# Kernel optimization log

Measured on AMD Instinct MI355X. Metric: run time of the kernel, lower is better.

## Reference

```python
import jax, jax.numpy as jnp
import numpy as np
import math

D_MODEL = 2048
N_HEADS = 16
HEAD_DIM = D_MODEL // N_HEADS  # 128
SEQ = 2048
BATCH = 1


def make_freqs(seq_len, head_dim, theta=10000.0):
    # standard rotary frequencies: freqs_cis = exp(i * t * inv_freq)
    inv_freq = 1.0 / (theta ** (np.arange(0, head_dim, 2, dtype=np.float32) / head_dim))
    t = np.arange(seq_len, dtype=np.float32)
    ang = np.outer(t, inv_freq)  # [seq, head_dim/2]
    return jnp.asarray(np.cos(ang)), jnp.asarray(np.sin(ang))


def setup_inputs() -> dict:
    key = jax.random.key(0)
    ks = jax.random.split(key, 6)
    x = jax.random.normal(ks[0], (BATCH, SEQ, D_MODEL), dtype=jnp.float32)
    freqs_cos, freqs_sin = make_freqs(SEQ, HEAD_DIM)
    # causal additive mask, broadcastable to [b, h, s, s]
    mask = jnp.where(jnp.tril(jnp.ones((SEQ, SEQ), dtype=bool)), 0.0, -1e9).astype(jnp.float32)[None, None]
    scale = 0.02
    wq = jax.random.normal(ks[1], (D_MODEL, D_MODEL), dtype=jnp.float32) * scale
    wk = jax.random.normal(ks[2], (D_MODEL, D_MODEL), dtype=jnp.float32) * scale
    wv = jax.random.normal(ks[3], (D_MODEL, D_MODEL), dtype=jnp.float32) * scale
    wo = jax.random.normal(ks[4], (D_MODEL, D_MODEL), dtype=jnp.float32) * scale
    return {"x": x, "freqs_cos": freqs_cos, "freqs_sin": freqs_sin, "mask": mask,
            "wq": wq, "wk": wk, "wv": wv, "wo": wo}


def _apply_rotary(q, k, cos, sin):
    # q, k: [b, s, h, hd]; cos/sin: [s, hd/2]
    def rot(t):
        tr = t.reshape(*t.shape[:-1], -1, 2)  # [b, s, h, hd/2, 2]
        re, im = tr[..., 0], tr[..., 1]
        c = cos[None, :, None, :]
        s = sin[None, :, None, :]
        # complex multiply (re + i im) * (c + i s)
        out_re = re * c - im * s
        out_im = re * s + im * c
        return jnp.stack([out_re, out_im], axis=-1).reshape(t.shape)
    return rot(q), rot(k)


def reference(x, freqs_cos, freqs_sin, mask, wq, wk, wv, wo):
    b, s, _ = x.shape
    # QKV projections (nn.Linear with no bias: x @ W^T; W is square so use x @ W
    # with W stored already-transposed -- weights here are random so x @ W is faithful math)
    q = (x @ wq).reshape(b, s, N_HEADS, HEAD_DIM)
    k = (x @ wk).reshape(b, s, N_HEADS, HEAD_DIM)
    v = (x @ wv).reshape(b, s, N_HEADS, HEAD_DIM)
    q, k = _apply_rotary(q, k, freqs_cos, freqs_sin)
    # [b, h, s_q, s_k]
    scores = jnp.einsum("bqhd,bkhd->bhqk", q, k) / math.sqrt(HEAD_DIM)
    scores = scores + mask
    probs = jax.nn.softmax(scores.astype(jnp.float32), axis=-1).astype(q.dtype)
    out = jnp.einsum("bhqk,bkhd->bqhd", probs, v).reshape(b, s, N_HEADS * HEAD_DIM)
    return out @ wo
```

## Files before the change

### kernel.cpp

```cpp
#include <hip/hip_runtime.h>
#include <hip/hip_bf16.h>
#include <math.h>

#define SEQ 2048
#define DM 2048
#define NH 16
#define HD 128
#define QKV_N 6144

typedef __bf16 bf16;
typedef __bf16 bf16x8 __attribute__((ext_vector_type(8)));
typedef __bf16 bf16x4v __attribute__((ext_vector_type(4)));
typedef __bf16 bf16x2v __attribute__((ext_vector_type(2)));
typedef float f32x4 __attribute__((ext_vector_type(4)));

__device__ inline int sw_idx32(int row, int quad) {
    return (row * 4 + (quad ^ ((row >> 1) & 3))) * 8;
}
__device__ inline int sw_idx64(int row, int chunk) {
    return (row * 8 + (chunk ^ (row & 7))) * 8;
}

__device__ inline void async16(const void* g, void* l) {
    __builtin_amdgcn_global_load_lds((const __attribute__((address_space(1))) void*)g,
                                     (__attribute__((address_space(3))) void*)l, 16, 0, 0);
}

__global__ void k_prep(const float* __restrict__ wq, const float* __restrict__ wk,
                       const float* __restrict__ wv, const float* __restrict__ wo,
                       bf16* __restrict__ wT, bf16* __restrict__ woT,
                       const float* __restrict__ x, bf16* __restrict__ xb) {
    const int z = blockIdx.z;
    int tx = threadIdx.x, ty = threadIdx.y;
    if (z == 4) {
        int bid = blockIdx.y * 64 + blockIdx.x;
        if (bid >= 1024) return;
        int i = bid * 1024 + ty * 32 + tx;
        float4 v = ((const float4*)x)[i];
        bf16x4v o;
        o.x = (bf16)v.x; o.y = (bf16)v.y; o.z = (bf16)v.z; o.w = (bf16)v.w;
        ((bf16x4v*)xb)[i] = o;
        return;
    }
    __shared__ float tile[32][33];
    const float* src = (z == 0) ? wq : (z == 1) ? wk : (z == 2) ? wv : wo;
    bf16* dst = (z < 3) ? (wT + (size_t)z * DM * DM) : woT;
    int bx = blockIdx.x * 32, by = blockIdx.y * 32;
    tile[ty][tx] = src[(size_t)(by + ty) * DM + bx + tx];
    __syncthreads();
    dst[(size_t)(bx + ty) * DM + by + tx] = (bf16)tile[tx][ty];
}

__global__ void k_post(bf16* __restrict__ qkv, const float* __restrict__ cosT,
                       const float* __restrict__ sinT, bf16* __restrict__ vT) {
    __shared__ bf16 tile[32][33];
    int tx = threadIdx.x, ty = threadIdx.y;
    if (blockIdx.y < 64) {
        int bx = blockIdx.x * 32, by = blockIdx.y * 32;
        tile[ty][tx] = qkv[(size_t)(by + ty) * QKV_N + 2 * DM + bx + tx];
        __syncthreads();
        vT[(size_t)(bx + ty) * SEQ + by + tx] = tile[tx][ty];
    } else {
        int b = (blockIdx.y - 64) * 64 + blockIdx.x;
        int idx = b * 1024 + ty * 32 + tx;
        int i = idx & 63;
        int h = (idx >> 6) & 15;
        int s = idx >> 10;
        float c = cosT[s * 64 + i], sn = sinT[s * 64 + i];
        size_t base = (size_t)s * QKV_N + h * HD + 2 * i;
        bf16x2v q = *(bf16x2v*)&qkv[base];
        float qr = (float)q.x, qi = (float)q.y;
        bf16x2v qo;
        qo.x = (bf16)(qr * c - qi * sn);
        qo.y = (bf16)(qr * sn + qi * c);
        *(bf16x2v*)&qkv[base] = qo;
        bf16x2v k = *(bf16x2v*)&qkv[base + DM];
        float kr = (float)k.x, ki = (float)k.y;
        bf16x2v ko;
        ko.x = (bf16)(kr * c - ki * sn);
        ko.y = (bf16)(kr * sn + ki * c);
        *(bf16x2v*)&qkv[base + DM] = ko;
    }
}

template <typename OutT, int KSPLIT>
__global__ __launch_bounds__(256) void k_gemm_bt(const bf16* __restrict__ A,
                                                 const bf16* __restrict__ Bt,
                                                 OutT* __restrict__ C,
                                                 int M, int N, int K) {
    __shared__ bf16 As[128 * 64];
    __shared__ bf16 Bs[128 * 64];
    const int t = threadIdx.x;
    const int lane = t & 63;
    const int w = t >> 6;
    const int wr = (w >> 1) * 64, wc = (w & 1) * 64;
    const int l15 = lane & 15, quad = lane >> 4;
    const size_t bm = (size_t)blockIdx.y * 128, bn = (size_t)blockIdx.x * 128;
    const int Kb = K / KSPLIT;
    const int k0 = (KSPLIT > 1) ? (int)blockIdx.z * Kb : 0;
    f32x4 acc[4][4];
#pragma unroll
    for (int i = 0; i < 4; ++i)
#pragma unroll
        for (int j = 0; j < 4; ++j) acc[i][j] = (f32x4){0.f, 0.f, 0.f, 0.f};

    int srow[4], sgc[4];
#pragma unroll
    for (int j = 0; j < 4; ++j) {
        int c = j * 256 + t;
        srow[j] = c >> 3;
        sgc[j] = ((c & 7) ^ (srow[j] & 7)) * 8;
    }

    for (int kt = 0; kt < Kb; kt += 64) {
#pragma unroll
        for (int j = 0; j < 4; ++j) {
            async16(&A[(bm + srow[j]) * K + k0 + kt + sgc[j]], &As[(j * 256 + t) * 8]);
            async16(&Bt[(bn + srow[j]) * K + k0 + kt + sgc[j]], &Bs[(j * 256 + t) * 8]);
        }
        __syncthreads();
#pragma unroll
        for (int kh = 0; kh < 2; ++kh) {
            bf16x8 af[4], bfm[4];
#pragma unroll
            for (int mi = 0; mi < 4; ++mi)
                af[mi] = *(const bf16x8*)&As[sw_idx64(wr + mi * 16 + l15, kh * 4 + quad)];
#pragma unroll
            for (int ni = 0; ni < 4; ++ni)
                bfm[ni] = *(const bf16x8*)&Bs[sw_idx64(wc + ni * 16 + l15, kh * 4 + quad)];
#pragma unroll
            for (int mi = 0; mi < 4; ++mi)
#pragma unroll
                for (int ni = 0; ni < 4; ++ni)
                    acc[mi][ni] = __builtin_amdgcn_mfma_f32_16x16x32_bf16(
                        af[mi], bfm[ni], acc[mi][ni], 0, 0, 0);
        }
        __syncthreads();
    }
#pragma unroll
    for (int mi = 0; mi < 4; ++mi)
#pragma unroll
        for (int ni = 0; ni < 4; ++ni)
#pragma unroll
            for (int r = 0; r < 4; ++r) {
                size_t row = bm + wr + mi * 16 + quad * 4 + r;
                size_t col = bn + wc + ni * 16 + l15;
                if (KSPLIT > 1)
                    unsafeAtomicAdd((float*)&C[row * (size_t)N + col],
                                    (float)acc[mi][ni][r]);
                else
                    C[row * (size_t)N + col] = (OutT)acc[mi][ni][r];
            }
}

__global__ __launch_bounds__(256) void k_flash(const bf16* __restrict__ qkv,
                                               const bf16* __restrict__ vT,
                                               bf16* __restrict__ out) {
    __shared__ bf16 Ks[4][64 * 32];
    __shared__ bf16 Vs[2][128 * 32];
    __shared__ bf16 Pl[4][16][72];
    const int t = threadIdx.x;
    const int lane = t & 63;
    const int w = t >> 6;
    const int l15 = lane & 15, quad = lane >> 4;
    const int b = blockIdx.x;
    const int h = (b & 7) * 2 + ((b >> 3) & 1);
    const int qb = 31 - (b >> 4);
    const int q0w = qb * 64 + w * 16;
    const float sc = 0.08838834764831845f;

    const size_t qrow = (size_t)(q0w + l15) * QKV_N + h * HD;
    bf16x8 aq[4];
#pragma unroll
    for (int u = 0; u < 4; ++u)
        aq[u] = *(const bf16x8*)&qkv[qrow + u * 32 + quad * 8];

    f32x4 o[8];
#pragma unroll
    for (int c = 0; c < 8; ++c) o[c] = (f32x4){0.f, 0.f, 0.f, 0.f};
    float l_r[4] = {0.f, 0.f, 0.f, 0.f};

    const int srow = t >> 2;
    const int ch = ((t & 3) ^ ((t >> 3) & 3)) * 8;

    for (int kt = 0; kt <= qb; ++kt) {
        const int kbase = kt * 64;
#pragma unroll
        for (int u = 0; u < 4; ++u)
            async16(&qkv[(size_t)(kbase + srow) * QKV_N + DM + h * HD + u * 32 + ch],
                    &Ks[u][t * 8]);
#pragma unroll
        for (int j = 0; j < 2; ++j) {
            async16(&vT[(size_t)(h * HD + srow) * SEQ + kbase + j * 32 + ch],
                    &Vs[j][t * 8]);
            async16(&vT[(size_t)(h * HD + 64 + srow) * SEQ + kbase + j * 32 + ch],
                    &Vs[j][(t + 256) * 8]);
        }
        __syncthreads();
        f32x4 s[4];
#pragma unroll
        for (int sub = 0; sub < 4; ++sub) {
            f32x4 z = (f32x4){0.f, 0.f, 0.f, 0.f};
#pragma unroll
            for (int u = 0; u < 4; ++u) {
                bf16x8 kb = *(const bf16x8*)&Ks[u][sw_idx32(sub * 16 + l15, quad)];
                z = __builtin_amdgcn_mfma_f32_16x16x32_bf16(aq[u], kb, z, 0, 0, 0);
            }
            s[sub] = z;
        }
        const bool masked = (kt == qb);
#pragma unroll
        for (int sub = 0; sub < 4; ++sub)
#pragma unroll
            for (int r = 0; r < 4; ++r) {
                float p = __expf(s[sub][r] * sc);
                if (masked)
                    p = (kbase + sub * 16 + l15 <= q0w + quad * 4 + r) ? p : 0.f;
                l_r[r] += p;
                Pl[w][quad * 4 + r][sub * 16 + l15] = (bf16)p;
            }
        __syncthreads();
        bf16x8 pf0 = *(const bf16x8*)&Pl[w][l15][quad * 8];
        bf16x8 pf1 = *(const bf16x8*)&Pl[w][l15][32 + quad * 8];
#pragma unroll
        for (int c = 0; c < 8; ++c) {
            bf16x8 vb0 = *(const bf16x8*)&Vs[0][sw_idx32(c * 16 + l15, quad)];
            o[c] = __builtin_amdgcn_mfma_f32_16x16x32_bf16(pf0, vb0, o[c], 0, 0, 0);
            bf16x8 vb1 = *(const bf16x8*)&Vs[1][sw_idx32(c * 16 + l15, quad)];
            o[c] = __builtin_amdgcn_mfma_f32_16x16x32_bf16(pf1, vb1, o[c], 0, 0, 0);
        }
        __syncthreads();
    }

    float rl[4];
#pragma unroll
    for (int r = 0; r < 4; ++r) {
        float l = l_r[r];
        l += __shfl_xor(l, 1, 16);
        l += __shfl_xor(l, 2, 16);
        l += __shfl_xor(l, 4, 16);
        l += __shfl_xor(l, 8, 16);
        rl[r] = 1.0f / l;
    }
#pragma unroll
    for (int c = 0; c < 8; ++c)
#pragma unroll
        for (int r = 0; r < 4; ++r)
            out[(size_t)(q0w + quad * 4 + r) * DM + h * HD + c * 16 + l15] =
                (bf16)(o[c][r] * rl[r]);
}

extern "C" void kernel_launch(void* const* d_in, const int* in_sizes, int n_in,
                              void* d_out, int out_size, void* d_ws, size_t ws_size,
                              hipStream_t stream) {
    const float* x  = (const float*)d_in[0];
    const float* fc = (const float*)d_in[1];
    const float* fs = (const float*)d_in[2];
    const float* wq = (const float*)d_in[4];
    const float* wk = (const float*)d_in[5];
    const float* wv = (const float*)d_in[6];
    const float* wo = (const float*)d_in[7];
    float* out = (float*)d_out;

    char* ws = (char*)d_ws;
    bf16* xb  = (bf16*)(ws);
    bf16* wT  = (bf16*)(ws + (size_t)(8u  << 20));
    bf16* woT = (bf16*)(ws + (size_t)(32u << 20));
    bf16* qkv = (bf16*)(ws + (size_t)(40u << 20));
    bf16* vT  = (bf16*)(ws + (size_t)(64u << 20));

    hipMemsetAsync(out, 0, (size_t)SEQ * DM * sizeof(float), stream);
    k_prep<<<dim3(64, 64, 5), dim3(32, 32), 0, stream>>>(wq, wk, wv, wo, wT, woT, x, xb);
    k_gemm_bt<bf16, 1><<<dim3(48, 16), 256, 0, stream>>>(xb, wT, qkv, SEQ, QKV_N, DM);
    k_post<<<dim3(64, 96), dim3(32, 32), 0, stream>>>(qkv, fc, fs, vT);
    k_flash<<<512, 256, 0, stream>>>(qkv, vT, xb);
    k_gemm_bt<float, 2><<<dim3(16, 16, 2), 256, 0, stream>>>(xb, woT, out, SEQ, DM, DM);
}
```

Measured before the change: 331.1 us.

## Fuse rotary and V transpose into QKV GEMM epilogue; drop split-K output GEMM

The QKV projection GEMM now applies rotary embedding to Q/K in its epilogue, pairing adjacent columns with a lane shuffle. It also writes V transposed through a swizzled LDS staging tile, which removes the separate k_post kernel and its extra pass over qkv. The output projection drops split-K with atomics and the memset in favour of a 128x64 tile with direct stores and more blocks. In exchange the epilogue is heavier, and the output GEMM does a full-K loop per block with less reuse.

```diff
diff --git a/kernel.cpp b/kernel.cpp
--- a/kernel.cpp
+++ b/kernel.cpp
@@ -51,53 +51,22 @@
     dst[(size_t)(bx + ty) * DM + by + tx] = (bf16)tile[tx][ty];
 }
 
-__global__ void k_post(bf16* __restrict__ qkv, const float* __restrict__ cosT,
-                       const float* __restrict__ sinT, bf16* __restrict__ vT) {
-    __shared__ bf16 tile[32][33];
-    int tx = threadIdx.x, ty = threadIdx.y;
-    if (blockIdx.y < 64) {
-        int bx = blockIdx.x * 32, by = blockIdx.y * 32;
-        tile[ty][tx] = qkv[(size_t)(by + ty) * QKV_N + 2 * DM + bx + tx];
-        __syncthreads();
-        vT[(size_t)(bx + ty) * SEQ + by + tx] = tile[tx][ty];
-    } else {
-        int b = (blockIdx.y - 64) * 64 + blockIdx.x;
-        int idx = b * 1024 + ty * 32 + tx;
-        int i = idx & 63;
-        int h = (idx >> 6) & 15;
-        int s = idx >> 10;
-        float c = cosT[s * 64 + i], sn = sinT[s * 64 + i];
-        size_t base = (size_t)s * QKV_N + h * HD + 2 * i;
-        bf16x2v q = *(bf16x2v*)&qkv[base];
-        float qr = (float)q.x, qi = (float)q.y;
-        bf16x2v qo;
-        qo.x = (bf16)(qr * c - qi * sn);
-        qo.y = (bf16)(qr * sn + qi * c);
-        *(bf16x2v*)&qkv[base] = qo;
-        bf16x2v k = *(bf16x2v*)&qkv[base + DM];
-        float kr = (float)k.x, ki = (float)k.y;
-        bf16x2v ko;
-        ko.x = (bf16)(kr * c - ki * sn);
-        ko.y = (bf16)(kr * sn + ki * c);
-        *(bf16x2v*)&qkv[base + DM] = ko;
-    }
-}
-
-template <typename OutT, int KSPLIT>
-__global__ __launch_bounds__(256) void k_gemm_bt(const bf16* __restrict__ A,
-                                                 const bf16* __restrict__ Bt,
-                                                 OutT* __restrict__ C,
-                                                 int M, int N, int K) {
-    __shared__ bf16 As[128 * 64];
-    __shared__ bf16 Bs[128 * 64];
+__global__ __launch_bounds__(256) void k_gemm_qkv(const bf16* __restrict__ A,
+                                                  const bf16* __restrict__ Bt,
+                                                  bf16* __restrict__ qkv,
+                                                  bf16* __restrict__ vT,
+                                                  const float* __restrict__ cosT,
+                                                  const float* __restrict__ sinT) {
+    const int K = DM;
+    __shared__ bf16 smem[2 * 128 * 64];
+    bf16* As = smem;
+    bf16* Bs = smem + 128 * 64;
     const int t = threadIdx.x;
     const int lane = t & 63;
     const int w = t >> 6;
     const int wr = (w >> 1) * 64, wc = (w & 1) * 64;
     const int l15 = lane & 15, quad = lane >> 4;
     const size_t bm = (size_t)blockIdx.y * 128, bn = (size_t)blockIdx.x * 128;
-    const int Kb = K / KSPLIT;
-    const int k0 = (KSPLIT > 1) ? (int)blockIdx.z * Kb : 0;
     f32x4 acc[4][4];
 #pragma unroll
     for (int i = 0; i < 4; ++i)
@@ -112,11 +81,11 @@
         sgc[j] = ((c & 7) ^ (srow[j] & 7)) * 8;
     }
 
-    for (int kt = 0; kt < Kb; kt += 64) {
+    for (int kt = 0; kt < K; kt += 64) {
 #pragma unroll
         for (int j = 0; j < 4; ++j) {
-            async16(&A[(bm + srow[j]) * K + k0 + kt + sgc[j]], &As[(j * 256 + t) * 8]);
-            async16(&Bt[(bn + srow[j]) * K + k0 + kt + sgc[j]], &Bs[(j * 256 + t) * 8]);
+            async16(&A[(bm + srow[j]) * K + kt + sgc[j]], &As[(j * 256 + t) * 8]);
+            async16(&Bt[(bn + srow[j]) * K + kt + sgc[j]], &Bs[(j * 256 + t) * 8]);
         }
         __syncthreads();
 #pragma unroll
@@ -137,19 +106,112 @@
         }
         __syncthreads();
     }
+
+    if (blockIdx.x < 32) {
+        const bool is_re = (l15 & 1) == 0;
+#pragma unroll
+        for (int mi = 0; mi < 4; ++mi)
+#pragma unroll
+            for (int ni = 0; ni < 4; ++ni) {
+                const int n_local = wc + ni * 16 + l15;
+                const int i = n_local >> 1;
+#pragma unroll
+                for (int r = 0; r < 4; ++r) {
+                    size_t row = bm + wr + mi * 16 + quad * 4 + r;
+                    float c = cosT[row * 64 + i];
+                    float sn = sinT[row * 64 + i];
+                    float a = acc[mi][ni][r];
+                    float p = __shfl_xor(a, 1);
+                    float v = is_re ? (a * c - p * sn) : (p * sn + a * c);
+                    qkv[row * QKV_N + bn + n_local] = (bf16)v;
+                }
+            }
+    } else {
+#pragma unroll
+        for (int mi = 0; mi < 4; ++mi)
+#pragma unroll
+            for (int ni = 0; ni < 4; ++ni) {
+                const int n_local = wc + ni * 16 + l15;
+#pragma unroll
+                for (int r = 0; r < 4; ++r) {
+                    int s_local = wr + mi * 16 + quad * 4 + r;
+                    smem[n_local * 128 + ((((s_local >> 3) ^ (n_local & 15)) * 8) |
+                                          (s_local & 7))] = (bf16)acc[mi][ni][r];
+                }
+            }
+        __syncthreads();
+        const int n_l = t >> 1;
+        const size_t ch = bn - 4096 + n_l;
+#pragma unroll
+        for (int j = 0; j < 8; ++j) {
+            int c = (t & 1) * 8 + j;
+            bf16x8 v = *(const bf16x8*)&smem[n_l * 128 + ((c ^ (n_l & 15)) * 8)];
+            *(bf16x8*)&vT[ch * SEQ + bm + c * 8] = v;
+        }
+    }
+}
+
+template <typename OutT, int BN>
+__global__ __launch_bounds__(256) void k_gemm_bt(const bf16* __restrict__ A,
+                                                 const bf16* __restrict__ Bt,
+                                                 OutT* __restrict__ C,
+                                                 int M, int N, int K) {
+    constexpr int NI = BN / 32;
+    __shared__ bf16 As[128 * 64];
+    __shared__ bf16 Bs[BN * 64];
+    const int t = threadIdx.x;
+    const int lane = t & 63;
+    const int w = t >> 6;
+    const int wr = (w >> 1) * 64, wc = (w & 1) * (BN / 2);
+    const int l15 = lane & 15, quad = lane >> 4;
+    const size_t bm = (size_t)blockIdx.y * 128, bn = (size_t)blockIdx.x * BN;
+    f32x4 acc[4][NI];
+#pragma unroll
+    for (int i = 0; i < 4; ++i)
+#pragma unroll
+        for (int j = 0; j < NI; ++j) acc[i][j] = (f32x4){0.f, 0.f, 0.f, 0.f};
+
+    for (int kt = 0; kt < K; kt += 64) {
+#pragma unroll
+        for (int j = 0; j < 4; ++j) {
+            int c = j * 256 + t;
+            int row = c >> 3, g = ((c & 7) ^ (row & 7)) * 8;
+            async16(&A[(bm + row) * K + kt + g], &As[c * 8]);
+        }
+#pragma unroll
+        for (int j = 0; j < NI; ++j) {
+            int c = j * 256 + t;
+            int row = c >> 3, g = ((c & 7) ^ (row & 7)) * 8;
+            async16(&Bt[(bn + row) * K + kt + g], &Bs[c * 8]);
+        }
+        __syncthreads();
+#pragma unroll
+        for (int kh = 0; kh < 2; ++kh) {
+            bf16x8 af[4], bfm[NI];
+#pragma unroll
+            for (int mi = 0; mi < 4; ++mi)
+                af[mi] = *(const bf16x8*)&As[sw_idx64(wr + mi * 16 + l15, kh * 4 + quad)];
+#pragma unroll
+            for (int ni = 0; ni < NI; ++ni)
+                bfm[ni] = *(const bf16x8*)&Bs[sw_idx64(wc + ni * 16 + l15, kh * 4 + quad)];
+#pragma unroll
+            for (int mi = 0; mi < 4; ++mi)
+#pragma unroll
+                for (int ni = 0; ni < NI; ++ni)
+                    acc[mi][ni] = __builtin_amdgcn_mfma_f32_16x16x32_bf16(
+                        af[mi], bfm[ni], acc[mi][ni], 0, 0, 0);
+        }
+        __syncthreads();
+    }
 #pragma unroll
     for (int mi = 0; mi < 4; ++mi)
 #pragma unroll
-        for (int ni = 0; ni < 4; ++ni)
+        for (int ni = 0; ni < NI; ++ni)
 #pragma unroll
             for (int r = 0; r < 4; ++r) {
                 size_t row = bm + wr + mi * 16 + quad * 4 + r;
                 size_t col = bn + wc + ni * 16 + l15;
-                if (KSPLIT > 1)
-                    unsafeAtomicAdd((float*)&C[row * (size_t)N + col],
-                                    (float)acc[mi][ni][r]);
-                else
-                    C[row * (size_t)N + col] = (OutT)acc[mi][ni][r];
+                C[row * (size_t)N + col] = (OutT)acc[mi][ni][r];
             }
 }
 
@@ -269,10 +331,8 @@
     bf16* qkv = (bf16*)(ws + (size_t)(40u << 20));
     bf16* vT  = (bf16*)(ws + (size_t)(64u << 20));
 
-    hipMemsetAsync(out, 0, (size_t)SEQ * DM * sizeof(float), stream);
     k_prep<<<dim3(64, 64, 5), dim3(32, 32), 0, stream>>>(wq, wk, wv, wo, wT, woT, x, xb);
-    k_gemm_bt<bf16, 1><<<dim3(48, 16), 256, 0, stream>>>(xb, wT, qkv, SEQ, QKV_N, DM);
-    k_post<<<dim3(64, 96), dim3(32, 32), 0, stream>>>(qkv, fc, fs, vT);
+    k_gemm_qkv<<<dim3(48, 16), 256, 0, stream>>>(xb, wT, qkv, vT, fc, fs);
     k_flash<<<512, 256, 0, stream>>>(qkv, vT, xb);
-    k_gemm_bt<float, 2><<<dim3(16, 16, 2), 256, 0, stream>>>(xb, woT, out, SEQ, DM, DM);
-}
+    k_gemm_bt<float, 64><<<dim3(32, 16), 256, 0, stream>>>(xb, woT, out, SEQ, DM, DM);
+}
```

Result: no change. 327.7 us (-1.0%).

## Widen flash KV tile to 128 and drop split-K atomics in output GEMM

Applied to the files above, without the earlier changes.

The attention kernel now stages 128 keys and values per iteration in XOR-swizzled LDS tiles, which halves the number of loop trips and block-wide barriers. The block barrier between writing P and reading it is replaced by an LDS waitcnt, since each wave only reads its own P rows. The output projection drops split-K atomics and the memset, using a narrower 128x64 tile with plain stores instead. The trade-off is a much larger LDS footprint in the flash kernel (about 80KB), which can lower occupancy, and more work is spent on the masked diagonal tile.

```diff
diff --git a/kernel.cpp b/kernel.cpp
--- a/kernel.cpp
+++ b/kernel.cpp
@@ -14,11 +14,11 @@
 typedef __bf16 bf16x2v __attribute__((ext_vector_type(2)));
 typedef float f32x4 __attribute__((ext_vector_type(4)));
 
-__device__ inline int sw_idx32(int row, int quad) {
-    return (row * 4 + (quad ^ ((row >> 1) & 3))) * 8;
-}
 __device__ inline int sw_idx64(int row, int chunk) {
     return (row * 8 + (chunk ^ (row & 7))) * 8;
+}
+__device__ inline int sw_idx128(int row, int chunk) {
+    return (row * 16 + (chunk ^ (row & 15))) * 8;
 }
 
 __device__ inline void async16(const void* g, void* l) {
@@ -83,55 +83,53 @@
     }
 }
 
-template <typename OutT, int KSPLIT>
+template <typename OutT, int BN>
 __global__ __launch_bounds__(256) void k_gemm_bt(const bf16* __restrict__ A,
                                                  const bf16* __restrict__ Bt,
                                                  OutT* __restrict__ C,
                                                  int M, int N, int K) {
+    constexpr int NI = BN / 32;
     __shared__ bf16 As[128 * 64];
-    __shared__ bf16 Bs[128 * 64];
+    __shared__ bf16 Bs[BN * 64];
     const int t = threadIdx.x;
     const int lane = t & 63;
     const int w = t >> 6;
-    const int wr = (w >> 1) * 64, wc = (w & 1) * 64;
+    const int wr = (w >> 1) * 64, wc = (w & 1) * (BN / 2);
     const int l15 = lane & 15, quad = lane >> 4;
-    const size_t bm = (size_t)blockIdx.y * 128, bn = (size_t)blockIdx.x * 128;
-    const int Kb = K / KSPLIT;
-    const int k0 = (KSPLIT > 1) ? (int)blockIdx.z * Kb : 0;
-    f32x4 acc[4][4];
+    const size_t bm = (size_t)blockIdx.y * 128, bn = (size_t)blockIdx.x * BN;
+    f32x4 acc[4][NI];
 #pragma unroll
     for (int i = 0; i < 4; ++i)
 #pragma unroll
-        for (int j = 0; j < 4; ++j) acc[i][j] = (f32x4){0.f, 0.f, 0.f, 0.f};
-
-    int srow[4], sgc[4];
-#pragma unroll
-    for (int j = 0; j < 4; ++j) {
-        int c = j * 256 + t;
-        srow[j] = c >> 3;
-        sgc[j] = ((c & 7) ^ (srow[j] & 7)) * 8;
-    }
-
-    for (int kt = 0; kt < Kb; kt += 64) {
+        for (int j = 0; j < NI; ++j) acc[i][j] = (f32x4){0.f, 0.f, 0.f, 0.f};
+
+    for (int kt = 0; kt < K; kt += 64) {
 #pragma unroll
         for (int j = 0; j < 4; ++j) {
-            async16(&A[(bm + srow[j]) * K + k0 + kt + sgc[j]], &As[(j * 256 + t) * 8]);
-            async16(&Bt[(bn + srow[j]) * K + k0 + kt + sgc[j]], &Bs[(j * 256 + t) * 8]);
+            int c = j * 256 + t;
+            int row = c >> 3, g = ((c & 7) ^ (row & 7)) * 8;
+            async16(&A[(bm + row) * K + kt + g], &As[c * 8]);
+        }
+#pragma unroll
+        for (int j = 0; j < NI; ++j) {
+            int c = j * 256 + t;
+            int row = c >> 3, g = ((c & 7) ^ (row & 7)) * 8;
+            async16(&Bt[(bn + row) * K + kt + g], &Bs[c * 8]);
         }
         __syncthreads();
 #pragma unroll
         for (int kh = 0; kh < 2; ++kh) {
-            bf16x8 af[4], bfm[4];
+            bf16x8 af[4], bfm[NI];
 #pragma unroll
             for (int mi = 0; mi < 4; ++mi)
                 af[mi] = *(const bf16x8*)&As[sw_idx64(wr + mi * 16 + l15, kh * 4 + quad)];
 #pragma unroll
-            for (int ni = 0; ni < 4; ++ni)
+            for (int ni = 0; ni < NI; ++ni)
                 bfm[ni] = *(const bf16x8*)&Bs[sw_idx64(wc + ni * 16 + l15, kh * 4 + quad)];
 #pragma unroll
             for (int mi = 0; mi < 4; ++mi)
 #pragma unroll
-                for (int ni = 0; ni < 4; ++ni)
+                for (int ni = 0; ni < NI; ++ni)
                     acc[mi][ni] = __builtin_amdgcn_mfma_f32_16x16x32_bf16(
                         af[mi], bfm[ni], acc[mi][ni], 0, 0, 0);
         }
@@ -140,25 +138,21 @@
 #pragma unroll
     for (int mi = 0; mi < 4; ++mi)
 #pragma unroll
-        for (int ni = 0; ni < 4; ++ni)
+        for (int ni = 0; ni < NI; ++ni)
 #pragma unroll
             for (int r = 0; r < 4; ++r) {
                 size_t row = bm + wr + mi * 16 + quad * 4 + r;
                 size_t col = bn + wc + ni * 16 + l15;
-                if (KSPLIT > 1)
-                    unsafeAtomicAdd((float*)&C[row * (size_t)N + col],
-                                    (float)acc[mi][ni][r]);
-                else
-                    C[row * (size_t)N + col] = (OutT)acc[mi][ni][r];
+                C[row * (size_t)N + col] = (OutT)acc[mi][ni][r];
             }
 }
 
 __global__ __launch_bounds__(256) void k_flash(const bf16* __restrict__ qkv,
                                                const bf16* __restrict__ vT,
                                                bf16* __restrict__ out) {
-    __shared__ bf16 Ks[4][64 * 32];
-    __shared__ bf16 Vs[2][128 * 32];
-    __shared__ bf16 Pl[4][16][72];
+    __shared__ bf16 Ks[128 * 128];
+    __shared__ bf16 Vs[128 * 128];
+    __shared__ bf16 Pl[4][16 * 128];
     const int t = threadIdx.x;
     const int lane = t & 63;
     const int w = t >> 6;
@@ -180,55 +174,62 @@
     for (int c = 0; c < 8; ++c) o[c] = (f32x4){0.f, 0.f, 0.f, 0.f};
     float l_r[4] = {0.f, 0.f, 0.f, 0.f};
 
-    const int srow = t >> 2;
-    const int ch = ((t & 3) ^ ((t >> 3) & 3)) * 8;
-
-    for (int kt = 0; kt <= qb; ++kt) {
-        const int kbase = kt * 64;
-#pragma unroll
-        for (int u = 0; u < 4; ++u)
-            async16(&qkv[(size_t)(kbase + srow) * QKV_N + DM + h * HD + u * 32 + ch],
-                    &Ks[u][t * 8]);
-#pragma unroll
-        for (int j = 0; j < 2; ++j) {
-            async16(&vT[(size_t)(h * HD + srow) * SEQ + kbase + j * 32 + ch],
-                    &Vs[j][t * 8]);
-            async16(&vT[(size_t)(h * HD + 64 + srow) * SEQ + kbase + j * 32 + ch],
-                    &Vs[j][(t + 256) * 8]);
-        }
-        __syncthreads();
-        f32x4 s[4];
-#pragma unroll
-        for (int sub = 0; sub < 4; ++sub) {
+    int srow[8], sg[8];
+#pragma unroll
+    for (int j = 0; j < 8; ++j) {
+        int c = j * 256 + t;
+        srow[j] = c >> 4;
+        sg[j] = ((c & 15) ^ (srow[j] & 15)) * 8;
+    }
+
+    const int n128 = (qb + 2) >> 1;
+    for (int kt = 0; kt < n128; ++kt) {
+        const int kbase = kt * 128;
+#pragma unroll
+        for (int j = 0; j < 8; ++j)
+            async16(&qkv[(size_t)(kbase + srow[j]) * QKV_N + DM + h * HD + sg[j]],
+                    &Ks[(j * 256 + t) * 8]);
+#pragma unroll
+        for (int j = 0; j < 8; ++j)
+            async16(&vT[(size_t)(h * HD + srow[j]) * SEQ + kbase + sg[j]],
+                    &Vs[(j * 256 + t) * 8]);
+        __syncthreads();
+        f32x4 s[8];
+#pragma unroll
+        for (int sub = 0; sub < 8; ++sub) {
             f32x4 z = (f32x4){0.f, 0.f, 0.f, 0.f};
 #pragma unroll
             for (int u = 0; u < 4; ++u) {
-                bf16x8 kb = *(const bf16x8*)&Ks[u][sw_idx32(sub * 16 + l15, quad)];
+                bf16x8 kb = *(const bf16x8*)&Ks[sw_idx128(sub * 16 + l15, u * 4 + quad)];
                 z = __builtin_amdgcn_mfma_f32_16x16x32_bf16(aq[u], kb, z, 0, 0, 0);
             }
             s[sub] = z;
         }
-        const bool masked = (kt == qb);
-#pragma unroll
-        for (int sub = 0; sub < 4; ++sub)
+        const bool masked = (kt == n128 - 1);
+#pragma unroll
+        for (int sub = 0; sub < 8; ++sub)
 #pragma unroll
             for (int r = 0; r < 4; ++r) {
                 float p = __expf(s[sub][r] * sc);
                 if (masked)
                     p = (kbase + sub * 16 + l15 <= q0w + quad * 4 + r) ? p : 0.f;
                 l_r[r] += p;
-                Pl[w][quad * 4 + r][sub * 16 + l15] = (bf16)p;
-            }
-        __syncthreads();
-        bf16x8 pf0 = *(const bf16x8*)&Pl[w][l15][quad * 8];
-        bf16x8 pf1 = *(const bf16x8*)&Pl[w][l15][32 + quad * 8];
-#pragma unroll
-        for (int c = 0; c < 8; ++c) {
-            bf16x8 vb0 = *(const bf16x8*)&Vs[0][sw_idx32(c * 16 + l15, quad)];
-            o[c] = __builtin_amdgcn_mfma_f32_16x16x32_bf16(pf0, vb0, o[c], 0, 0, 0);
-            bf16x8 vb1 = *(const bf16x8*)&Vs[1][sw_idx32(c * 16 + l15, quad)];
-            o[c] = __builtin_amdgcn_mfma_f32_16x16x32_bf16(pf1, vb1, o[c], 0, 0, 0);
-        }
+                int rowp = quad * 4 + r;
+                int col = sub * 16 + l15;
+                Pl[w][rowp * 128 + ((col >> 3) ^ (rowp & 15)) * 8 + (col & 7)] = (bf16)p;
+            }
+        __asm__ __volatile__("s_waitcnt lgkmcnt(0)" ::: "memory");
+        bf16x8 pf[4];
+#pragma unroll
+        for (int kk = 0; kk < 4; ++kk)
+            pf[kk] = *(const bf16x8*)&Pl[w][sw_idx128(l15, kk * 4 + quad)];
+#pragma unroll
+        for (int c = 0; c < 8; ++c)
+#pragma unroll
+            for (int kk = 0; kk < 4; ++kk) {
+                bf16x8 vb = *(const bf16x8*)&Vs[sw_idx128(c * 16 + l15, kk * 4 + quad)];
+                o[c] = __builtin_amdgcn_mfma_f32_16x16x32_bf16(pf[kk], vb, o[c], 0, 0, 0);
+            }
         __syncthreads();
     }
 
@@ -269,10 +270,9 @@
     bf16* qkv = (bf16*)(ws + (size_t)(40u << 20));
     bf16* vT  = (bf16*)(ws + (size_t)(64u << 20));
 
-    hipMemsetAsync(out, 0, (size_t)SEQ * DM * sizeof(float), stream);
     k_prep<<<dim3(64, 64, 5), dim3(32, 32), 0, stream>>>(wq, wk, wv, wo, wT, woT, x, xb);
-    k_gemm_bt<bf16, 1><<<dim3(48, 16), 256, 0, stream>>>(xb, wT, qkv, SEQ, QKV_N, DM);
+    k_gemm_bt<bf16, 128><<<dim3(48, 16), 256, 0, stream>>>(xb, wT, qkv, SEQ, QKV_N, DM);
     k_post<<<dim3(64, 96), dim3(32, 32), 0, stream>>>(qkv, fc, fs, vT);
     k_flash<<<512, 256, 0, stream>>>(qkv, vT, xb);
-    k_gemm_bt<float, 2><<<dim3(16, 16, 2), 256, 0, stream>>>(xb, woT, out, SEQ, DM, DM);
-}
+    k_gemm_bt<float, 64><<<dim3(32, 16), 256, 0, stream>>>(xb, woT, out, SEQ, DM, DM);
+}
```

Result: faster. 311.8 us (-5.8%).
